# Kernel tuning notes

Hardware: AMD Instinct MI355X
Metric: run time of the kernel (lower is better)

## Reference

```python
import jax, jax.numpy as jnp
import numpy as np

NUM_BBOX = 2
NUM_CLASSES = 20
NUM_GRID = 7
THR_CONF = 0.5
THR_NMS = 0.3
BATCH = 128


def setup_inputs() -> dict:
    key = jax.random.key(0)
    C = NUM_BBOX * 4 + NUM_BBOX + NUM_CLASSES  # 30
    p = jax.random.normal(key, (BATCH, NUM_GRID, NUM_GRID, C), dtype=jnp.float32)
    return {"p_yolo_ts4": p}


def _decode(p):
    B, S = p.shape[0], p.shape[1]
    sc = NUM_BBOX * 4
    conf = jax.nn.sigmoid(p[..., sc:sc + NUM_BBOX])          # [B,S,S,nb] objectness
    cls = jax.nn.sigmoid(p[..., sc + NUM_BBOX:])             # [B,S,S,nc]
    boxes = p[..., :sc].reshape(B, S, S, NUM_BBOX, 4)
    xy = jax.nn.sigmoid(boxes[..., :2])                      # cell-relative offsets
    col = jnp.arange(S, dtype=p.dtype)
    cx = (xy[..., 0] + col[None, None, :, None]) / NUM_GRID  # + col index (x)
    cy = (xy[..., 1] + col[None, :, None, None]) / NUM_GRID  # + row index (y)
    w, h = boxes[..., 2], boxes[..., 3]                      # raw wh, as in source
    ltrb = jnp.stack([cx - w / 2, cy - h / 2, cx + w / 2, cy + h / 2], axis=-1)
    labels = jnp.argmax(cls, axis=-1) + 1                    # [B,S,S]
    valid = conf > THR_CONF                                  # [B,S,S,nb]
    return ltrb, conf, labels, valid


def _pairwise_iou(b):
    lt = jnp.maximum(b[:, None, :2], b[None, :, :2])
    rb = jnp.minimum(b[:, None, 2:], b[None, :, 2:])
    wh = jnp.clip(rb - lt, 0.0)
    inter = wh[..., 0] * wh[..., 1]
    area = (b[:, 2] - b[:, 0]) * (b[:, 3] - b[:, 1])
    union = area[:, None] + area[None, :] - inter
    return inter / jnp.maximum(union, 1e-9)


def reference(p_yolo_ts4):
    p = p_yolo_ts4
    B, S = p.shape[0], p.shape[1]
    ltrb, conf, labels, valid = _decode(p)
    N = B * S * S * NUM_BBOX
    boxes = ltrb.reshape(N, 4)
    scores = conf.reshape(N)
    labs = jnp.broadcast_to(labels[..., None], (B, S, S, NUM_BBOX)).reshape(N)
    idsb = jnp.broadcast_to(jnp.arange(B)[:, None, None, None], (B, S, S, NUM_BBOX)).reshape(N)
    vmask = valid.reshape(N)
    # sort by score (invalid last); greedy NMS per (batch, label) group
    order = jnp.argsort(jnp.where(vmask, scores, -jnp.inf))[::-1]
    boxes_s = boxes[order]
    scores_s = scores[order]
    labs_s = labs[order]
    idsb_s = idsb[order]
    v_s = vmask[order]
    iou = _pairwise_iou(boxes_s)                              # [N,N]
    same = (idsb_s[:, None] == idsb_s[None, :]) & (labs_s[:, None] == labs_s[None, :])
    later = jnp.arange(N)[None, :] > jnp.arange(N)[:, None]
    sup_mat = (iou > THR_NMS) & same & later & v_s[None, :]

    def body(i, sup):
        keep_i = v_s[i] & jnp.logical_not(sup[i])
        return jnp.where(keep_i, sup | sup_mat[i], sup)

    sup = jax.lax.fori_loop(0, N, body, jnp.zeros((N,), dtype=bool))
    keep = v_s & jnp.logical_not(sup)
    # fixed-shape outputs in descending-score order; `keep` marks surviving boxes
    return idsb_s, boxes_s, labs_s, scores_s, keep
```

## Files before the change

kernel.cpp:

```cpp
#include <hip/hip_runtime.h>
#include <math.h>

#define NBATCH 128
#define S 7
#define CH 30
#define N 12544
#define PERB 98
#define NWORDS 196
#define NBUCK 4096
#define MAXB 32
#define POISON 0xAAAAAAAAu
#define THRNMS 0.3
#define SCBASE 0x3F000000u

__device__ __forceinline__ float sigf(float x) {
    float e = (float)exp(-(double)x);
    return 1.0f / (1.0f + e);
}

__device__ __forceinline__ unsigned int bucket_of(unsigned int scb) {
    unsigned int bk = (scb - SCBASE) >> 11;
    return bk > (NBUCK - 1) ? (NBUCK - 1) : bk;
}

__global__ __launch_bounds__(64) void k_decode(
    const float* __restrict__ p,
    float4* __restrict__ box4,
    float* __restrict__ score,
    unsigned long long* __restrict__ vK,
    unsigned long long* __restrict__ ballots,
    unsigned int* __restrict__ hist,
    unsigned long long* __restrict__ bkeys)
{
    int i    = blockIdx.x * 64 + threadIdx.x;
    int lane = threadIdx.x;
    int j    = i & 1;
    int cell = i >> 1;
    int x = cell % S, y = (cell / S) % S;
    const float* pc = p + cell * CH;

    float tx = pc[j*4+0], ty = pc[j*4+1], tw = pc[j*4+2], th = pc[j*4+3];
    float craw = pc[8 + j];

    int cbase = 10 + j * 10;
    float best = pc[cbase]; int lab = j * 10;
    #pragma unroll
    for (int c = 1; c < 10; ++c) {
        float v = pc[cbase + c];
        if (v > best) { best = v; lab = j * 10 + c; }
    }
    float obest = __shfl_xor(best, 1);
    int   olab  = __shfl_xor(lab, 1);
    float bestA = j ? obest : best;  int labA = j ? olab : lab;
    float bestB = j ? best  : obest; int labB = j ? lab  : olab;
    int label = (bestB > bestA ? labB : labA) + 1;

    float sx = sigf(tx), sy = sigf(ty);
    float cx = (sx + (float)x) / 7.0f;
    float cy = (sy + (float)y) / 7.0f;
    float hw = tw / 2.0f, hh = th / 2.0f;
    float l = cx - hw, t = cy - hh, r = cx + hw, bt = cy + hh;

    float sc = sigf(craw);
    bool valid = sc > 0.5f;

    box4[i]  = make_float4(l, t, r, bt);
    score[i] = sc;

    unsigned int scb = __float_as_uint(sc);
    unsigned long long lowk = ((unsigned long long)(unsigned int)i << 7)
                            | (unsigned long long)(unsigned int)label;
    unsigned long long K = valid ? ((unsigned long long)scb << 32) | lowk : lowk;
    vK[i] = K;

    unsigned long long vb = __ballot(valid);
    if (lane == 0) ballots[i >> 6] = vb;

    if (valid) {
        unsigned int bk = bucket_of(scb);
        unsigned int slot = atomicAdd(&hist[bk], 1u) - POISON;
        if (slot < MAXB) bkeys[(bk << 5) | slot] = K;
    }
}

__global__ __launch_bounds__(256) void k_prefix(
    const unsigned int* __restrict__ hist,
    const unsigned long long* __restrict__ ballots,
    unsigned int* __restrict__ prefHigher,
    unsigned int* __restrict__ wpre)
{
    __shared__ unsigned int sc_[256];
    const int t = threadIdx.x;

    const uint4* hp = (const uint4*)hist;
    uint4 a0 = hp[t*4+0], a1 = hp[t*4+1], a2 = hp[t*4+2], a3 = hp[t*4+3];
    unsigned int v[16] = { a0.x, a0.y, a0.z, a0.w,  a1.x, a1.y, a1.z, a1.w,
                           a2.x, a2.y, a2.z, a2.w,  a3.x, a3.y, a3.z, a3.w };
    unsigned int pv[16], run = 0;
    #pragma unroll
    for (int k = 0; k < 16; ++k) { run += v[k] - POISON; pv[k] = run; }
    sc_[t] = run;
    __syncthreads();
    for (int off = 1; off < 256; off <<= 1) {
        unsigned int add = (t >= off) ? sc_[t - off] : 0u;
        __syncthreads();
        sc_[t] += add;
        __syncthreads();
    }
    unsigned int incl  = sc_[t];
    unsigned int total = sc_[255];
    unsigned int excl  = incl - run;
    #pragma unroll
    for (int k = 0; k < 16; ++k)
        prefHigher[t*16 + k] = total - (excl + pv[k]);
    __syncthreads();

    unsigned int pcv = 0;
    if (t < NWORDS) pcv = (unsigned int)__popcll(ballots[t]);
    sc_[t] = pcv;
    __syncthreads();
    for (int off = 1; off < 256; off <<= 1) {
        unsigned int add = (t >= off) ? sc_[t - off] : 0u;
        __syncthreads();
        sc_[t] += add;
        __syncthreads();
    }
    if (t < NWORDS) wpre[t] = sc_[t] - pcv;
}

__global__ __launch_bounds__(128) void k_finish(
    const unsigned long long* __restrict__ vK,
    const unsigned int* __restrict__ hist,
    const unsigned long long* __restrict__ bkeys,
    const unsigned int* __restrict__ prefHigher,
    const unsigned int* __restrict__ wpre,
    const unsigned long long* __restrict__ ballots,
    const float4* __restrict__ box4,
    const float* __restrict__ score,
    float* __restrict__ out)
{
    const int b   = blockIdx.x;
    const int tid = threadIdx.x;
    __shared__ unsigned long long mK[PERB];
    __shared__ float sbx[PERB][4];
    __shared__ int   slb[PERB], spos[PERB], sup[PERB];
    __shared__ float ssc[PERB];
    __shared__ unsigned int wcnt[2];

    const int gi = b * PERB + tid;
    bool isv = false;
    unsigned long long K = 0ull;
    float sc = 0.0f;
    float4 b4 = make_float4(0.f, 0.f, 0.f, 0.f);
    if (tid < PERB) {
        K  = vK[gi];
        sc = score[gi];
        b4 = box4[gi];
        isv = (K >> 32) != 0ull;
        mK[tid] = K;
    }
    unsigned long long vb = __ballot(isv);
    if ((tid & 63) == 0) wcnt[tid >> 6] = (unsigned int)__popcll(vb);
    __syncthreads();
    const int kb = (int)(wcnt[0] + wcnt[1]);

    if (tid < PERB) {
        int label = (int)(K & 0x7Full);
        if (isv) {
            unsigned int scb = (unsigned int)(K >> 32);
            unsigned int bk  = bucket_of(scb);
            unsigned int c   = hist[bk] - POISON;
            if (c > MAXB) c = MAXB;
            unsigned int cnt = 0;
            for (unsigned int u = 0; u < c; ++u)
                cnt += (bkeys[(bk << 5) + u] > K) ? 1u : 0u;
            unsigned int pos = prefHigher[bk] + cnt;

            int rk = 0;
            #pragma unroll
            for (int u = 0; u < PERB; ++u) rk += (mK[u] > K) ? 1 : 0;
            sbx[rk][0] = b4.x; sbx[rk][1] = b4.y; sbx[rk][2] = b4.z; sbx[rk][3] = b4.w;
            slb[rk]  = label;
            ssc[rk]  = sc;
            spos[rk] = (int)pos;
            sup[rk]  = 0;
        } else {
            unsigned int w = (unsigned int)gi >> 6;
            unsigned long long bw = ballots[w];
            unsigned int vle = wpre[w]
                + (unsigned int)__popcll(bw & ((1ull << (gi & 63)) - 1ull));
            unsigned int pos = (unsigned int)(N - 1 - gi) + vle;
            out[pos] = (float)b;
            ((float4*)(out + N))[pos] = b4;
            out[5*N + pos] = (float)label;
            out[6*N + pos] = sc;
            out[7*N + pos] = 0.0f;
        }
    }
    __syncthreads();

    for (int i = 0; i < kb; ++i) {
        __syncthreads();
        if (sup[i]) continue;
        float li = sbx[i][0], ti = sbx[i][1], ri = sbx[i][2], bi = sbx[i][3];
        float areai = (ri - li) * (bi - ti);
        int labi = slb[i];
        int jj = tid;
        if (jj > i && jj < kb && slb[jj] == labi) {
            float lj = sbx[jj][0], tj = sbx[jj][1], rj = sbx[jj][2], bj = sbx[jj][3];
            float lt0 = fmaxf(li, lj), lt1 = fmaxf(ti, tj);
            float rb0 = fminf(ri, rj), rb1 = fminf(bi, bj);
            float w = rb0 - lt0; if (w < 0.0f) w = 0.0f;
            float h = rb1 - lt1; if (h < 0.0f) h = 0.0f;
            float inter = w * h;
            float areaj = (rj - lj) * (bj - tj);
            float uni = areai + areaj - inter;
            double iou = (double)inter / fmax((double)uni, 1e-9);
            if (iou > THRNMS) sup[jj] = 1;
        }
    }
    __syncthreads();

    if (tid < kb) {
        int pos = spos[tid];
        out[pos] = (float)b;
        ((float4*)(out + N))[pos] =
            make_float4(sbx[tid][0], sbx[tid][1], sbx[tid][2], sbx[tid][3]);
        out[5*N + pos] = (float)slb[tid];
        out[6*N + pos] = ssc[tid];
        out[7*N + pos] = sup[tid] ? 0.0f : 1.0f;
    }
}

extern "C" void kernel_launch(void* const* d_in, const int* in_sizes, int n_in,
                              void* d_out, int out_size, void* d_ws, size_t ws_size,
                              hipStream_t stream)
{
    const float* p = (const float*)d_in[0];
    float* out = (float*)d_out;

    char* w = (char*)d_ws;
    float4* box4            = (float4*)w;             w += (size_t)N * 16;
    unsigned long long* vK  = (unsigned long long*)w; w += (size_t)N * 8;
    unsigned long long* bkeys = (unsigned long long*)w; w += (size_t)NBUCK * MAXB * 8;
    unsigned long long* ballots = (unsigned long long*)w; w += (size_t)NWORDS * 8;
    float* score            = (float*)w;              w += (size_t)N * 4;
    unsigned int* hist      = (unsigned int*)w;       w += (size_t)NBUCK * 4;
    unsigned int* prefHigher= (unsigned int*)w;       w += (size_t)NBUCK * 4;
    unsigned int* wpre      = (unsigned int*)w;       w += (size_t)NWORDS * 4;

    k_decode<<<dim3(N / 64), dim3(64),  0, stream>>>(p, box4, score, vK, ballots,
                                                     hist, bkeys);
    k_prefix<<<dim3(1),      dim3(256), 0, stream>>>(hist, ballots, prefHigher, wpre);
    k_finish<<<dim3(NBATCH), dim3(128), 0, stream>>>(vK, hist, bkeys, prefHigher, wpre,
                                                     ballots, box4, score, out);
}
```

Before: 74.85 us.

## Fuse prefix scan into finish kernel and use bitmask-based NMS

```diff
diff --git a/kernel.cpp b/kernel.cpp
--- a/kernel.cpp
+++ b/kernel.cpp
@@ -83,57 +83,10 @@
     }
 }
 
-__global__ __launch_bounds__(256) void k_prefix(
-    const unsigned int* __restrict__ hist,
-    const unsigned long long* __restrict__ ballots,
-    unsigned int* __restrict__ prefHigher,
-    unsigned int* __restrict__ wpre)
-{
-    __shared__ unsigned int sc_[256];
-    const int t = threadIdx.x;
-
-    const uint4* hp = (const uint4*)hist;
-    uint4 a0 = hp[t*4+0], a1 = hp[t*4+1], a2 = hp[t*4+2], a3 = hp[t*4+3];
-    unsigned int v[16] = { a0.x, a0.y, a0.z, a0.w,  a1.x, a1.y, a1.z, a1.w,
-                           a2.x, a2.y, a2.z, a2.w,  a3.x, a3.y, a3.z, a3.w };
-    unsigned int pv[16], run = 0;
-    #pragma unroll
-    for (int k = 0; k < 16; ++k) { run += v[k] - POISON; pv[k] = run; }
-    sc_[t] = run;
-    __syncthreads();
-    for (int off = 1; off < 256; off <<= 1) {
-        unsigned int add = (t >= off) ? sc_[t - off] : 0u;
-        __syncthreads();
-        sc_[t] += add;
-        __syncthreads();
-    }
-    unsigned int incl  = sc_[t];
-    unsigned int total = sc_[255];
-    unsigned int excl  = incl - run;
-    #pragma unroll
-    for (int k = 0; k < 16; ++k)
-        prefHigher[t*16 + k] = total - (excl + pv[k]);
-    __syncthreads();
-
-    unsigned int pcv = 0;
-    if (t < NWORDS) pcv = (unsigned int)__popcll(ballots[t]);
-    sc_[t] = pcv;
-    __syncthreads();
-    for (int off = 1; off < 256; off <<= 1) {
-        unsigned int add = (t >= off) ? sc_[t - off] : 0u;
-        __syncthreads();
-        sc_[t] += add;
-        __syncthreads();
-    }
-    if (t < NWORDS) wpre[t] = sc_[t] - pcv;
-}
-
 __global__ __launch_bounds__(128) void k_finish(
     const unsigned long long* __restrict__ vK,
     const unsigned int* __restrict__ hist,
     const unsigned long long* __restrict__ bkeys,
-    const unsigned int* __restrict__ prefHigher,
-    const unsigned int* __restrict__ wpre,
     const unsigned long long* __restrict__ ballots,
     const float4* __restrict__ box4,
     const float* __restrict__ score,
@@ -141,11 +94,67 @@
 {
     const int b   = blockIdx.x;
     const int tid = threadIdx.x;
+    __shared__ unsigned int prefH[NBUCK];
+    __shared__ unsigned int sc_[128];
+    __shared__ unsigned int wpre_[NWORDS];
     __shared__ unsigned long long mK[PERB];
     __shared__ float sbx[PERB][4];
-    __shared__ int   slb[PERB], spos[PERB], sup[PERB];
+    __shared__ int   slb[PERB], spos[PERB];
     __shared__ float ssc[PERB];
+    __shared__ unsigned long long msk[PERB][2];
+    __shared__ unsigned long long supw[2];
     __shared__ unsigned int wcnt[2];
+
+    {
+        const uint4* hp = (const uint4*)hist;
+        unsigned int v[32];
+        #pragma unroll
+        for (int q = 0; q < 8; ++q) {
+            uint4 a = hp[tid*8 + q];
+            v[q*4+0] = a.x - POISON; v[q*4+1] = a.y - POISON;
+            v[q*4+2] = a.z - POISON; v[q*4+3] = a.w - POISON;
+        }
+        unsigned int run = 0;
+        #pragma unroll
+        for (int k = 0; k < 32; ++k) { run += v[k]; v[k] = run; }
+        sc_[tid] = run;
+        __syncthreads();
+        for (int off = 1; off < 128; off <<= 1) {
+            unsigned int add = (tid >= off) ? sc_[tid - off] : 0u;
+            __syncthreads();
+            sc_[tid] += add;
+            __syncthreads();
+        }
+        unsigned int total = sc_[127];
+        unsigned int excl  = sc_[tid] - run;
+        #pragma unroll
+        for (int k = 0; k < 32; ++k)
+            prefH[tid*32 + k] = total - (excl + v[k]);
+    }
+    __syncthreads();
+
+    {
+        unsigned int p0 = 0, p1 = 0;
+        if (tid < 98) {
+            p0 = (unsigned int)__popcll(ballots[tid*2]);
+            p1 = (unsigned int)__popcll(ballots[tid*2+1]);
+        }
+        unsigned int s2 = p0 + p1;
+        sc_[tid] = s2;
+        __syncthreads();
+        for (int off = 1; off < 128; off <<= 1) {
+            unsigned int add = (tid >= off) ? sc_[tid - off] : 0u;
+            __syncthreads();
+            sc_[tid] += add;
+            __syncthreads();
+        }
+        if (tid < 98) {
+            unsigned int excl2 = sc_[tid] - s2;
+            wpre_[tid*2]   = excl2;
+            wpre_[tid*2+1] = excl2 + p0;
+        }
+    }
+    __syncthreads();
 
     const int gi = b * PERB + tid;
     bool isv = false;
@@ -174,7 +183,7 @@
             unsigned int cnt = 0;
             for (unsigned int u = 0; u < c; ++u)
                 cnt += (bkeys[(bk << 5) + u] > K) ? 1u : 0u;
-            unsigned int pos = prefHigher[bk] + cnt;
+            unsigned int pos = prefH[bk] + cnt;
 
             int rk = 0;
             #pragma unroll
@@ -183,11 +192,10 @@
             slb[rk]  = label;
             ssc[rk]  = sc;
             spos[rk] = (int)pos;
-            sup[rk]  = 0;
         } else {
             unsigned int w = (unsigned int)gi >> 6;
             unsigned long long bw = ballots[w];
-            unsigned int vle = wpre[w]
+            unsigned int vle = wpre_[w]
                 + (unsigned int)__popcll(bw & ((1ull << (gi & 63)) - 1ull));
             unsigned int pos = (unsigned int)(N - 1 - gi) + vle;
             out[pos] = (float)b;
@@ -199,36 +207,50 @@
     }
     __syncthreads();
 
-    for (int i = 0; i < kb; ++i) {
-        __syncthreads();
-        if (sup[i]) continue;
-        float li = sbx[i][0], ti = sbx[i][1], ri = sbx[i][2], bi = sbx[i][3];
+    if (tid < kb) {
+        float li = sbx[tid][0], ti = sbx[tid][1], ri = sbx[tid][2], bi = sbx[tid][3];
         float areai = (ri - li) * (bi - ti);
-        int labi = slb[i];
-        int jj = tid;
-        if (jj > i && jj < kb && slb[jj] == labi) {
-            float lj = sbx[jj][0], tj = sbx[jj][1], rj = sbx[jj][2], bj = sbx[jj][3];
-            float lt0 = fmaxf(li, lj), lt1 = fmaxf(ti, tj);
-            float rb0 = fminf(ri, rj), rb1 = fminf(bi, bj);
-            float w = rb0 - lt0; if (w < 0.0f) w = 0.0f;
-            float h = rb1 - lt1; if (h < 0.0f) h = 0.0f;
-            float inter = w * h;
-            float areaj = (rj - lj) * (bj - tj);
-            float uni = areai + areaj - inter;
-            double iou = (double)inter / fmax((double)uni, 1e-9);
-            if (iou > THRNMS) sup[jj] = 1;
-        }
+        int labi = slb[tid];
+        unsigned long long m0 = 0ull, m1 = 0ull;
+        for (int u = 0; u < kb; ++u) {
+            if (u > tid && slb[u] == labi) {
+                float lj = sbx[u][0], tj = sbx[u][1], rj = sbx[u][2], bj = sbx[u][3];
+                float lt0 = fmaxf(li, lj), lt1 = fmaxf(ti, tj);
+                float rb0 = fminf(ri, rj), rb1 = fminf(bi, bj);
+                float w = rb0 - lt0; if (w < 0.0f) w = 0.0f;
+                float h = rb1 - lt1; if (h < 0.0f) h = 0.0f;
+                float inter = w * h;
+                float areaj = (rj - lj) * (bj - tj);
+                float uni = areai + areaj - inter;
+                double iou = (double)inter / fmax((double)uni, 1e-9);
+                if (iou > THRNMS) {
+                    if (u < 64) m0 |= 1ull << u; else m1 |= 1ull << (u - 64);
+                }
+            }
+        }
+        msk[tid][0] = m0; msk[tid][1] = m1;
+    }
+    __syncthreads();
+    if (tid == 0) {
+        unsigned long long s0 = 0ull, s1 = 0ull;
+        for (int i = 0; i < kb; ++i) {
+            bool su = (i < 64) ? ((s0 >> i) & 1ull) : ((s1 >> (i - 64)) & 1ull);
+            if (!su) { s0 |= msk[i][0]; s1 |= msk[i][1]; }
+        }
+        supw[0] = s0; supw[1] = s1;
     }
     __syncthreads();
 
     if (tid < kb) {
         int pos = spos[tid];
+        bool su = (tid < 64) ? ((supw[0] >> tid) & 1ull)
+                             : ((supw[1] >> (tid - 64)) & 1ull);
         out[pos] = (float)b;
         ((float4*)(out + N))[pos] =
             make_float4(sbx[tid][0], sbx[tid][1], sbx[tid][2], sbx[tid][3]);
         out[5*N + pos] = (float)slb[tid];
         out[6*N + pos] = ssc[tid];
-        out[7*N + pos] = sup[tid] ? 0.0f : 1.0f;
+        out[7*N + pos] = su ? 0.0f : 1.0f;
     }
 }
 
@@ -246,12 +268,9 @@
     unsigned long long* ballots = (unsigned long long*)w; w += (size_t)NWORDS * 8;
     float* score            = (float*)w;              w += (size_t)N * 4;
     unsigned int* hist      = (unsigned int*)w;       w += (size_t)NBUCK * 4;
-    unsigned int* prefHigher= (unsigned int*)w;       w += (size_t)NBUCK * 4;
-    unsigned int* wpre      = (unsigned int*)w;       w += (size_t)NWORDS * 4;
 
     k_decode<<<dim3(N / 64), dim3(64),  0, stream>>>(p, box4, score, vK, ballots,
                                                      hist, bkeys);
-    k_prefix<<<dim3(1),      dim3(256), 0, stream>>>(hist, ballots, prefHigher, wpre);
-    k_finish<<<dim3(NBATCH), dim3(128), 0, stream>>>(vK, hist, bkeys, prefHigher, wpre,
-                                                     ballots, box4, score, out);
-}
+    k_finish<<<dim3(NBATCH), dim3(128), 0, stream>>>(vK, hist, bkeys, ballots,
+                                                     box4, score, out);
+}
```

Result: no change. 74.24 us (-0.8%).
